# Kernel optimization log

Hardware: AMD Instinct MI355X
Metric: run time of the kernel (lower is better)

The kernel has to match this reference:

```python
import jax, jax.numpy as jnp
import numpy as np

B, S, D, H = 64, 512, 512, 1024


def setup_inputs() -> dict:
    key = jax.random.key(0)
    ks = jax.random.split(key, 18)
    p = {}
    p["inputs"] = jax.random.normal(ks[0], (B, S, D), jnp.float32)
    p["H0"] = jax.random.normal(ks[1], (B, H), jnp.float32)
    p["C0"] = jax.random.normal(ks[2], (B, H), jnp.float32)
    INIT_STD = 0.01  # nn.initializers.normal() default stddev
    for j, n in enumerate(["i", "f", "o", "c"]):
        p[f"Wx{n}"] = INIT_STD * jax.random.normal(ks[3 + 3 * j], (D, H), jnp.float32)
        p[f"Wh{n}"] = INIT_STD * jax.random.normal(ks[4 + 3 * j], (H, H), jnp.float32)
        p[f"b{n}"] = jnp.zeros((H,), jnp.float32)
    # flax Dense default: lecun_normal kernel, zeros bias
    p["fc_W"] = jax.random.normal(ks[15], (H, 1), jnp.float32) / np.float32(np.sqrt(H))
    p["fc_b"] = jnp.zeros((1,), jnp.float32)
    return p


def _lstm_forward(inputs, H0, C0, Wxi, Whi, bi, Wxf, Whf, bf,
                  Wxo, Who, bo, Wxc, Whc, bc, fc_W, fc_b):
    # Fuse the 4 gate weight matrices: same math, one GEMM per source.
    Wx = jnp.concatenate([Wxi, Wxf, Wxo, Wxc], axis=1)  # [D, 4H]
    Wh = jnp.concatenate([Whi, Whf, Who, Whc], axis=1)  # [H, 4H]
    b = jnp.concatenate([bi, bf, bo, bc], axis=0)       # [4H]
    # Precompute input projections for all timesteps: [S, B, 4H]
    x_proj = jnp.einsum('bsd,dg->sbg', inputs, Wx) + b

    def step(carry, xp):
        Hs, Cs = carry
        g = xp + Hs @ Wh                       # [B, 4H]
        i, f, o, c = jnp.split(g, 4, axis=-1)
        i = jax.nn.sigmoid(i)
        f = jax.nn.sigmoid(f)
        o = jax.nn.sigmoid(o)
        c = jnp.tanh(c)
        Cn = f * Cs + i * c
        Hn = o * jnp.tanh(Cn)
        return (Hn, Cn), Hn

    (Hf, Cf), outs = jax.lax.scan(step, (H0, C0), x_proj)
    outputs = jnp.transpose(outs, (1, 0, 2))   # [B, S, H]
    pred = outputs @ fc_W + fc_b               # [B, S, 1]
    return pred, Hf, Cf


def reference(inputs, H0, C0, Wxi, Whi, bi, Wxf, Whf, bf,
              Wxo, Who, bo, Wxc, Whc, bc, fc_W, fc_b):
    return _lstm_forward(inputs, H0, C0, Wxi, Whi, bi, Wxf, Whf, bf,
                         Wxo, Who, bo, Wxc, Whc, bc, fc_W, fc_b)
```

## Files before the change

### kernel.cpp

```cpp
#include <hip/hip_runtime.h>

typedef unsigned short u16;
typedef __bf16 bf16x8 __attribute__((ext_vector_type(8)));
typedef float f32x4 __attribute__((ext_vector_type(4)));

#define NWG 256

__device__ __forceinline__ u16 f2bf(float f) {
  union { float f; unsigned u; } v; v.f = f;
  unsigned r = v.u + 0x7fffu + ((v.u >> 16) & 1u);
  return (u16)(r >> 16);
}
__device__ __forceinline__ float bf2f(u16 h) {
  union { unsigned u; float f; } v; v.u = ((unsigned)h) << 16;
  return v.f;
}
__device__ __forceinline__ float fsig(float x) { return 1.0f / (1.0f + __expf(-x)); }
__device__ __forceinline__ float ftanh(float x) {
  float a = fabsf(x);
  float e = __expf(2.0f * a);
  float t = 1.0f - 2.0f / (e + 1.0f);
  return copysignf(t, x);
}

__global__ __launch_bounds__(256) void k_cvt_in(const float* __restrict__ inp,
                                                u16* __restrict__ dst) {
  unsigned i = blockIdx.x * 256 + threadIdx.x;
  unsigned d8 = i & 63u;
  unsigned b = (i >> 6) & 63u;
  unsigned s = i >> 12;
  const float* src = inp + ((size_t)b * 512 + s) * 512 + (size_t)d8 * 8;
  float4 x0 = *(const float4*)src;
  float4 x1 = *(const float4*)(src + 4);
  union { u16 h[8]; uint4 v; } o;
  o.h[0] = f2bf(x0.x); o.h[1] = f2bf(x0.y); o.h[2] = f2bf(x0.z); o.h[3] = f2bf(x0.w);
  o.h[4] = f2bf(x1.x); o.h[5] = f2bf(x1.y); o.h[6] = f2bf(x1.z); o.h[7] = f2bf(x1.w);
  *(uint4*)(dst + ((size_t)s * 64 + b) * 512 + d8 * 8) = o.v;
}

__global__ __launch_bounds__(256) void k_cvt_w(const float* __restrict__ W0,
                                               const float* __restrict__ W1,
                                               const float* __restrict__ W2,
                                               const float* __restrict__ W3,
                                               int K, u16* __restrict__ dst) {
  unsigned i = blockIdx.x * 256 + threadIdx.x;
  unsigned kb = (unsigned)K >> 3;
  unsigned k8 = i % kb;
  unsigned n = i / kb;
  if (n >= 4096) return;
  unsigned gate = n >> 10, h = n & 1023u;
  const float* W = (gate == 0) ? W0 : (gate == 1) ? W1 : (gate == 2) ? W2 : W3;
  union { u16 hh[8]; uint4 v; } o;
#pragma unroll
  for (int q = 0; q < 8; ++q) o.hh[q] = f2bf(W[(size_t)(k8 * 8 + q) * 1024 + h]);
  *(uint4*)(dst + (size_t)n * K + k8 * 8) = o.v;
}

__global__ __launch_bounds__(256) void k_init(const float* __restrict__ H0,
                                              u16* __restrict__ hbuf,
                                              unsigned* __restrict__ bar) {
  unsigned i = blockIdx.x * 256 + threadIdx.x;
  if (i < 16384) bar[i] = 0u;
  if (i < 65536) hbuf[i] = f2bf(H0[i]);
}

__global__ __launch_bounds__(256) void k_xp(const u16* __restrict__ A,
                                            const u16* __restrict__ Bm,
                                            u16* __restrict__ Xp) {
  __shared__ u16 Al[64][72];
  __shared__ u16 Bl[64][72];
  int t = threadIdx.x;
  int lane = t & 63, wid = t >> 6;
  int m0 = blockIdx.x * 64, n0 = blockIdx.y * 64;
  int quad = lane >> 4, l15 = lane & 15;
  f32x4 acc[4];
#pragma unroll
  for (int i = 0; i < 4; ++i) acc[i] = (f32x4){0.f, 0.f, 0.f, 0.f};
  int srow = t >> 2, sk = (t & 3) * 16;
  for (int kc = 0; kc < 512; kc += 64) {
    const u16* s1 = A + (size_t)(m0 + srow) * 512 + kc + sk;
    *(uint4*)&Al[srow][sk] = *(const uint4*)s1;
    *(uint4*)&Al[srow][sk + 8] = *(const uint4*)(s1 + 8);
    const u16* s2 = Bm + (size_t)(n0 + srow) * 512 + kc + sk;
    *(uint4*)&Bl[srow][sk] = *(const uint4*)s2;
    *(uint4*)&Bl[srow][sk + 8] = *(const uint4*)(s2 + 8);
    __syncthreads();
#pragma unroll
    for (int ks = 0; ks < 64; ks += 32) {
      bf16x8 a = *(const bf16x8*)&Al[wid * 16 + l15][ks + quad * 8];
#pragma unroll
      for (int nt = 0; nt < 4; ++nt) {
        bf16x8 b = *(const bf16x8*)&Bl[nt * 16 + l15][ks + quad * 8];
        acc[nt] = __builtin_amdgcn_mfma_f32_16x16x32_bf16(a, b, acc[nt], 0, 0, 0);
      }
    }
    __syncthreads();
  }
#pragma unroll
  for (int nt = 0; nt < 4; ++nt)
#pragma unroll
    for (int r = 0; r < 4; ++r) {
      size_t row = (size_t)m0 + wid * 16 + quad * 4 + r;
      Xp[row * 4096 + n0 + nt * 16 + l15] = f2bf(acc[nt][r]);
    }
}

__global__ __launch_bounds__(512, 2) void k_recur(
    u16* hbuf, const u16* __restrict__ whc, const u16* __restrict__ wxc,
    const u16* xp, const u16* inpb, const float* __restrict__ C0,
    const float* __restrict__ bi, const float* __restrict__ bff,
    const float* __restrict__ bo, const float* __restrict__ bc,
    float* __restrict__ dout, unsigned* bar, int use_xp) {
  int t = threadIdx.x;
  int wg = blockIdx.x;
  int lane = t & 63;
  int wid = t >> 6;
  int kset = wid >> 2;
  int wm = wid & 3;
  int h0 = wg << 2;
  int quad = lane >> 4;
  int ncol = lane & 15;

  unsigned* flags = bar;

  __shared__ u16 wxl[16][520];
  __shared__ float gt[2][4][16][17];
  __shared__ float biasl[16];

  int gate = ncol >> 2, j = ncol & 3;
  size_t colg = (size_t)gate * 1024 + h0 + j;
  bf16x8 wreg[16];
  {
    const u16* wb = whc + colg * 1024 + kset * 512 + quad * 8;
#pragma unroll
    for (int kk = 0; kk < 16; ++kk) wreg[kk] = *(const bf16x8*)(wb + kk * 32);
  }
  if (!use_xp) {
    int n = t >> 5;
    int part = t & 31;
    int g2 = n >> 2, j2n = n & 3;
    size_t cg = (size_t)g2 * 1024 + h0 + j2n;
    const u16* src2 = wxc + cg * 512 + part * 16;
#pragma unroll
    for (int q = 0; q < 2; ++q)
      *(uint4*)&wxl[n][part * 16 + q * 8] = *(const uint4*)(src2 + q * 8);
  }
  if (t < 16) {
    int g3 = t >> 2, j3 = t & 3;
    const float* bp = (g3 == 0) ? bi : (g3 == 1) ? bff : (g3 == 2) ? bo : bc;
    biasl[t] = bp[h0 + j3];
  }
  float Creg0 = 0.f, Creg1 = 0.f;
  if (t < 128) {
    int b = t >> 1, j2 = (t & 1) * 2;
    Creg0 = C0[b * 1024 + h0 + j2];
    Creg1 = C0[b * 1024 + h0 + j2 + 1];
  }

  int brow = wm * 16 + ncol;

  u16 xn0 = 0, xn1 = 0, xn2 = 0, xn3 = 0;
  const u16* xpc = 0;
  if (use_xp) {
    xpc = xp + (size_t)(wm * 16 + quad * 4) * 4096 + gate * 1024 + h0 + j;
    if (kset == 0) {
      xn0 = xpc[0]; xn1 = xpc[4096]; xn2 = xpc[8192]; xn3 = xpc[12288];
    }
  }
  __syncthreads();

  for (int s = 0; s < 512; ++s) {
    f32x4 acc = (f32x4){0.f, 0.f, 0.f, 0.f};
    f32x4 acc2 = (f32x4){0.f, 0.f, 0.f, 0.f};
    const u16* hrow = hbuf + (size_t)s * 65536 + (size_t)brow * 1024 + kset * 512;
    if (use_xp) {
      if (kset == 0) {
        acc[0] = bf2f(xn0); acc[1] = bf2f(xn1);
        acc[2] = bf2f(xn2); acc[3] = bf2f(xn3);
      }
    } else {
      const u16* irow = inpb + (size_t)s * 32768 + (size_t)brow * 512;
#pragma unroll
      for (int kk = 0; kk < 8; ++kk) {
        int kb = kset * 256 + kk * 32 + quad * 8;
        bf16x8 a = *(const bf16x8*)(irow + kb);
        bf16x8 w = *(const bf16x8*)&wxl[ncol][kb];
        acc = __builtin_amdgcn_mfma_f32_16x16x32_bf16(a, w, acc, 0, 0, 0);
      }
    }
#pragma unroll
    for (int kk = 0; kk < 16; ++kk) {
      bf16x8 a = *(const bf16x8*)(hrow + kk * 32 + quad * 8);
      if (kk & 1)
        acc2 = __builtin_amdgcn_mfma_f32_16x16x32_bf16(a, wreg[kk], acc2, 0, 0, 0);
      else
        acc = __builtin_amdgcn_mfma_f32_16x16x32_bf16(a, wreg[kk], acc, 0, 0, 0);
    }
    acc += acc2;
#pragma unroll
    for (int r = 0; r < 4; ++r)
      gt[kset][wm][quad * 4 + r][ncol] = acc[r];
    __syncthreads();
    if (t < 128) {
      int b = t >> 1, j2 = (t & 1) * 2;
      int m = b & 15, w2 = b >> 4;
      float Hn[2], Cn[2];
#pragma unroll
      for (int e = 0; e < 2; ++e) {
        int jj = j2 + e;
        float gi = gt[0][w2][m][jj] + gt[1][w2][m][jj] + biasl[jj];
        float gf = gt[0][w2][m][4 + jj] + gt[1][w2][m][4 + jj] + biasl[4 + jj];
        float go_ = gt[0][w2][m][8 + jj] + gt[1][w2][m][8 + jj] + biasl[8 + jj];
        float gc = gt[0][w2][m][12 + jj] + gt[1][w2][m][12 + jj] + biasl[12 + jj];
        float iv = fsig(gi), fv = fsig(gf), ov = fsig(go_), cv = ftanh(gc);
        float Cp = e ? Creg1 : Creg0;
        Cn[e] = fv * Cp + iv * cv;
        Hn[e] = ov * ftanh(Cn[e]);
      }
      Creg0 = Cn[0];
      Creg1 = Cn[1];
      unsigned pack = (unsigned)f2bf(Hn[0]) | ((unsigned)f2bf(Hn[1]) << 16);
      unsigned* hp = (unsigned*)(hbuf + (size_t)(s + 1) * 65536 + b * 1024 + h0 + j2);
      __hip_atomic_store(hp, pack, __ATOMIC_RELAXED, __HIP_MEMORY_SCOPE_AGENT);
      if (s == 511) {
        dout[32768 + b * 1024 + h0 + j2] = Hn[0];
        dout[32768 + b * 1024 + h0 + j2 + 1] = Hn[1];
        dout[98304 + b * 1024 + h0 + j2] = Cn[0];
        dout[98304 + b * 1024 + h0 + j2 + 1] = Cn[1];
      }
    }
    unsigned s1 = (unsigned)(s + 1);
    __syncthreads();
    if (s1 < 512) {
      if (t == 0)
        __hip_atomic_store(&flags[wg * 32], s1, __ATOMIC_RELAXED,
                           __HIP_MEMORY_SCOPE_AGENT);
      if (use_xp && kset == 0) {
        const u16* xpp = xpc + (size_t)s1 * 262144;
        xn0 = xpp[0]; xn1 = xpp[4096]; xn2 = xpp[8192]; xn3 = xpp[12288];
      }
      __asm__ volatile("" ::: "memory");
      if (t < 256) {
        while (__hip_atomic_load(&flags[t * 32], __ATOMIC_RELAXED,
                                 __HIP_MEMORY_SCOPE_AGENT) < s1)
          __builtin_amdgcn_s_sleep(2);
      }
      __syncthreads();
    }
  }
}

__global__ __launch_bounds__(256) void k_pred(const u16* __restrict__ hbuf,
                                              const float* __restrict__ fcW,
                                              const float* __restrict__ fcb,
                                              float* __restrict__ out) {
  __shared__ float w[1024];
  int t = threadIdx.x;
#pragma unroll
  for (int i = 0; i < 4; ++i) w[t + i * 256] = fcW[t + i * 256];
  __syncthreads();
  int wid = t >> 6, lane = t & 63;
  int row = blockIdx.x * 4 + wid;
  int b = row >> 9, s = row & 511;
  const u16* h = hbuf + (size_t)(s + 1) * 65536 + (size_t)b * 1024;
  float sum = 0.f;
#pragma unroll
  for (int it = 0; it < 16; ++it) {
    int hh = it * 64 + lane;
    sum += bf2f(h[hh]) * w[hh];
  }
#pragma unroll
  for (int o = 32; o > 0; o >>= 1) sum += __shfl_down(sum, o, 64);
  if (lane == 0) out[row] = sum + fcb[0];
}

extern "C" void kernel_launch(void* const* d_in, const int* in_sizes, int n_in,
                              void* d_out, int out_size, void* d_ws, size_t ws_size,
                              hipStream_t stream) {
  const float* inputs = (const float*)d_in[0];
  const float* H0 = (const float*)d_in[1];
  const float* C0 = (const float*)d_in[2];
  const float* Wxi = (const float*)d_in[3];
  const float* Whi = (const float*)d_in[4];
  const float* bi = (const float*)d_in[5];
  const float* Wxf = (const float*)d_in[6];
  const float* Whf = (const float*)d_in[7];
  const float* bff = (const float*)d_in[8];
  const float* Wxo = (const float*)d_in[9];
  const float* Who = (const float*)d_in[10];
  const float* bo = (const float*)d_in[11];
  const float* Wxc = (const float*)d_in[12];
  const float* Whc = (const float*)d_in[13];
  const float* bc = (const float*)d_in[14];
  const float* fcW = (const float*)d_in[15];
  const float* fcb = (const float*)d_in[16];
  float* out = (float*)d_out;

  char* ws = (char*)d_ws;
  size_t off = 0;
  auto take = [&](size_t bytes) {
    char* p = ws + off;
    off += (bytes + 255) & ~(size_t)255;
    return p;
  };
  unsigned* bar = (unsigned*)take(16384 * 4);
  u16* inpb = (u16*)take((size_t)512 * 64 * 512 * 2);
  u16* wxcT = (u16*)take((size_t)4096 * 512 * 2);
  u16* whcT = (u16*)take((size_t)4096 * 1024 * 2);
  u16* hbuf = (u16*)take((size_t)513 * 64 * 1024 * 2);
  u16* xpb = (u16*)take((size_t)32768 * 4096 * 2);
  size_t needA = off;
  int useA = (ws_size >= needA) ? 1 : 0;

  k_cvt_in<<<8192, 256, 0, stream>>>(inputs, inpb);
  k_cvt_w<<<1024, 256, 0, stream>>>(Wxi, Wxf, Wxo, Wxc, 512, wxcT);
  k_cvt_w<<<2048, 256, 0, stream>>>(Whi, Whf, Who, Whc, 1024, whcT);
  k_init<<<256, 256, 0, stream>>>(H0, hbuf, bar);
  if (useA) k_xp<<<dim3(512, 64), 256, 0, stream>>>(inpb, wxcT, xpb);
  k_recur<<<NWG, 512, 0, stream>>>(hbuf, whcT, wxcT, xpb, inpb, C0, bi, bff, bo,
                                   bc, out, bar, useA);
  k_pred<<<8192, 256, 0, stream>>>(hbuf, fcW, fcb, out);
}
```

Measured before the change: 4.062 ms.

## Split recurrence into batch groups with per-group barriers and full-K per wave

Repartitions the recurrent kernel so each group of 32 workgroups owns 8 batch rows, and each wave holds the full-K slice of Wh for 4 hidden columns in registers. Gate sums are no longer split across two K halves, so the intra-block syncthreads before the cell update is dropped and each wave does its own cell update. The cross-workgroup barrier now waits only on the 32 workgroups in the same batch group instead of all 256. The trade-off is half of each MFMA tile wasted (only 8 of 16 rows used), more weight registers per lane, and the use_xp flag becoming a template parameter.

```diff
diff --git a/kernel.cpp b/kernel.cpp
--- a/kernel.cpp
+++ b/kernel.cpp
@@ -105,129 +105,120 @@
     }
 }
 
+template <int USE_XP>
 __global__ __launch_bounds__(512, 2) void k_recur(
     u16* hbuf, const u16* __restrict__ whc, const u16* __restrict__ wxc,
     const u16* xp, const u16* inpb, const float* __restrict__ C0,
     const float* __restrict__ bi, const float* __restrict__ bff,
     const float* __restrict__ bo, const float* __restrict__ bc,
-    float* __restrict__ dout, unsigned* bar, int use_xp) {
+    float* __restrict__ dout, unsigned* bar) {
   int t = threadIdx.x;
   int wg = blockIdx.x;
+  int g = wg >> 5;
+  int wgi = wg & 31;
   int lane = t & 63;
-  int wid = t >> 6;
-  int kset = wid >> 2;
-  int wm = wid & 3;
-  int h0 = wg << 2;
+  int w = t >> 6;
   int quad = lane >> 4;
   int ncol = lane & 15;
+  int gate = ncol >> 2, hcl = ncol & 3;
+  int hc0 = wgi * 32 + w * 4;
 
   unsigned* flags = bar;
 
-  __shared__ u16 wxl[16][520];
-  __shared__ float gt[2][4][16][17];
-  __shared__ float biasl[16];
-
-  int gate = ncol >> 2, j = ncol & 3;
-  size_t colg = (size_t)gate * 1024 + h0 + j;
-  bf16x8 wreg[16];
+  __shared__ float gt[8][8][17];
+  __shared__ float biasl[8][16];
+
+  int n = gate * 1024 + hc0 + hcl;
+  bf16x8 wreg[32];
   {
-    const u16* wb = whc + colg * 1024 + kset * 512 + quad * 8;
-#pragma unroll
-    for (int kk = 0; kk < 16; ++kk) wreg[kk] = *(const bf16x8*)(wb + kk * 32);
-  }
-  if (!use_xp) {
-    int n = t >> 5;
-    int part = t & 31;
-    int g2 = n >> 2, j2n = n & 3;
-    size_t cg = (size_t)g2 * 1024 + h0 + j2n;
-    const u16* src2 = wxc + cg * 512 + part * 16;
-#pragma unroll
-    for (int q = 0; q < 2; ++q)
-      *(uint4*)&wxl[n][part * 16 + q * 8] = *(const uint4*)(src2 + q * 8);
-  }
-  if (t < 16) {
-    int g3 = t >> 2, j3 = t & 3;
-    const float* bp = (g3 == 0) ? bi : (g3 == 1) ? bff : (g3 == 2) ? bo : bc;
-    biasl[t] = bp[h0 + j3];
-  }
-  float Creg0 = 0.f, Creg1 = 0.f;
-  if (t < 128) {
-    int b = t >> 1, j2 = (t & 1) * 2;
-    Creg0 = C0[b * 1024 + h0 + j2];
-    Creg1 = C0[b * 1024 + h0 + j2 + 1];
-  }
-
-  int brow = wm * 16 + ncol;
+    const u16* wb = whc + (size_t)n * 1024 + quad * 8;
+#pragma unroll
+    for (int ks = 0; ks < 32; ++ks) wreg[ks] = *(const bf16x8*)(wb + ks * 32);
+  }
+  bf16x8 wxreg[USE_XP ? 1 : 16];
+  if (!USE_XP) {
+    const u16* wb2 = wxc + (size_t)n * 512 + quad * 8;
+#pragma unroll
+    for (int ks = 0; ks < 16; ++ks) wxreg[ks] = *(const bf16x8*)(wb2 + ks * 32);
+  }
+  if (lane < 16) {
+    const float* bp = (gate == 0) ? bi : (gate == 1) ? bff : (gate == 2) ? bo : bc;
+    biasl[w][lane] = bp[hc0 + hcl];
+  }
+  int bl = (lane & 31) >> 2, jcl = lane & 3;
+  int bg = 8 * g + bl;
+  int hcg = hc0 + jcl;
+  float Creg = 0.f;
+  if (lane < 32) Creg = C0[bg * 1024 + hcg];
+
+  int ba = 8 * g + (ncol & 7);
 
   u16 xn0 = 0, xn1 = 0, xn2 = 0, xn3 = 0;
   const u16* xpc = 0;
-  if (use_xp) {
-    xpc = xp + (size_t)(wm * 16 + quad * 4) * 4096 + gate * 1024 + h0 + j;
-    if (kset == 0) {
+  if (USE_XP) {
+    xpc = xp + (size_t)(8 * g + quad * 4) * 4096 + n;
+    if (quad < 2) {
       xn0 = xpc[0]; xn1 = xpc[4096]; xn2 = xpc[8192]; xn3 = xpc[12288];
     }
   }
   __syncthreads();
 
+  const u16* hrow = hbuf + (size_t)ba * 1024 + quad * 8;
   for (int s = 0; s < 512; ++s) {
     f32x4 acc = (f32x4){0.f, 0.f, 0.f, 0.f};
     f32x4 acc2 = (f32x4){0.f, 0.f, 0.f, 0.f};
-    const u16* hrow = hbuf + (size_t)s * 65536 + (size_t)brow * 1024 + kset * 512;
-    if (use_xp) {
-      if (kset == 0) {
+    if (USE_XP) {
+      if (quad < 2) {
         acc[0] = bf2f(xn0); acc[1] = bf2f(xn1);
         acc[2] = bf2f(xn2); acc[3] = bf2f(xn3);
       }
     } else {
-      const u16* irow = inpb + (size_t)s * 32768 + (size_t)brow * 512;
-#pragma unroll
-      for (int kk = 0; kk < 8; ++kk) {
-        int kb = kset * 256 + kk * 32 + quad * 8;
-        bf16x8 a = *(const bf16x8*)(irow + kb);
-        bf16x8 w = *(const bf16x8*)&wxl[ncol][kb];
-        acc = __builtin_amdgcn_mfma_f32_16x16x32_bf16(a, w, acc, 0, 0, 0);
-      }
-    }
-#pragma unroll
-    for (int kk = 0; kk < 16; ++kk) {
-      bf16x8 a = *(const bf16x8*)(hrow + kk * 32 + quad * 8);
-      if (kk & 1)
-        acc2 = __builtin_amdgcn_mfma_f32_16x16x32_bf16(a, wreg[kk], acc2, 0, 0, 0);
+      const u16* irow = inpb + (size_t)s * 32768 + (size_t)ba * 512 + quad * 8;
+#pragma unroll
+      for (int ks = 0; ks < 16; ++ks) {
+        bf16x8 a = *(const bf16x8*)(irow + ks * 32);
+        if (ks & 1)
+          acc2 = __builtin_amdgcn_mfma_f32_16x16x32_bf16(a, wxreg[ks], acc2, 0, 0, 0);
+        else
+          acc = __builtin_amdgcn_mfma_f32_16x16x32_bf16(a, wxreg[ks], acc, 0, 0, 0);
+      }
+    }
+#pragma unroll
+    for (int ks = 0; ks < 32; ++ks) {
+      bf16x8 a = *(const bf16x8*)(hrow + ks * 32);
+      if (ks & 1)
+        acc2 = __builtin_amdgcn_mfma_f32_16x16x32_bf16(a, wreg[ks], acc2, 0, 0, 0);
       else
-        acc = __builtin_amdgcn_mfma_f32_16x16x32_bf16(a, wreg[kk], acc, 0, 0, 0);
+        acc = __builtin_amdgcn_mfma_f32_16x16x32_bf16(a, wreg[ks], acc, 0, 0, 0);
     }
     acc += acc2;
-#pragma unroll
-    for (int r = 0; r < 4; ++r)
-      gt[kset][wm][quad * 4 + r][ncol] = acc[r];
-    __syncthreads();
-    if (t < 128) {
-      int b = t >> 1, j2 = (t & 1) * 2;
-      int m = b & 15, w2 = b >> 4;
-      float Hn[2], Cn[2];
-#pragma unroll
-      for (int e = 0; e < 2; ++e) {
-        int jj = j2 + e;
-        float gi = gt[0][w2][m][jj] + gt[1][w2][m][jj] + biasl[jj];
-        float gf = gt[0][w2][m][4 + jj] + gt[1][w2][m][4 + jj] + biasl[4 + jj];
-        float go_ = gt[0][w2][m][8 + jj] + gt[1][w2][m][8 + jj] + biasl[8 + jj];
-        float gc = gt[0][w2][m][12 + jj] + gt[1][w2][m][12 + jj] + biasl[12 + jj];
-        float iv = fsig(gi), fv = fsig(gf), ov = fsig(go_), cv = ftanh(gc);
-        float Cp = e ? Creg1 : Creg0;
-        Cn[e] = fv * Cp + iv * cv;
-        Hn[e] = ov * ftanh(Cn[e]);
-      }
-      Creg0 = Cn[0];
-      Creg1 = Cn[1];
-      unsigned pack = (unsigned)f2bf(Hn[0]) | ((unsigned)f2bf(Hn[1]) << 16);
-      unsigned* hp = (unsigned*)(hbuf + (size_t)(s + 1) * 65536 + b * 1024 + h0 + j2);
+    hrow += 65536;
+    if (quad < 2) {
+#pragma unroll
+      for (int r = 0; r < 4; ++r) gt[w][quad * 4 + r][ncol] = acc[r];
+    }
+    float Hn = 0.f, Cn = 0.f;
+    if (lane < 32) {
+      float gi = gt[w][bl][jcl] + biasl[w][jcl];
+      float gf = gt[w][bl][4 + jcl] + biasl[w][4 + jcl];
+      float go_ = gt[w][bl][8 + jcl] + biasl[w][8 + jcl];
+      float gc = gt[w][bl][12 + jcl] + biasl[w][12 + jcl];
+      float iv = fsig(gi), fv = fsig(gf), ov = fsig(go_), cv = ftanh(gc);
+      Cn = fv * Creg + iv * cv;
+      Creg = Cn;
+      Hn = ov * ftanh(Cn);
+    }
+    unsigned hb = (unsigned)f2bf(Hn);
+    unsigned up = (unsigned)__shfl_down((int)hb, 1, 64);
+    if (lane < 32 && (jcl & 1) == 0) {
+      unsigned pack = hb | (up << 16);
+      unsigned* hp =
+          (unsigned*)(hbuf + (size_t)(s + 1) * 65536 + bg * 1024 + hcg);
       __hip_atomic_store(hp, pack, __ATOMIC_RELAXED, __HIP_MEMORY_SCOPE_AGENT);
-      if (s == 511) {
-        dout[32768 + b * 1024 + h0 + j2] = Hn[0];
-        dout[32768 + b * 1024 + h0 + j2 + 1] = Hn[1];
-        dout[98304 + b * 1024 + h0 + j2] = Cn[0];
-        dout[98304 + b * 1024 + h0 + j2 + 1] = Cn[1];
-      }
+    }
+    if (s == 511 && lane < 32) {
+      dout[32768 + bg * 1024 + hcg] = Hn;
+      dout[98304 + bg * 1024 + hcg] = Cn;
     }
     unsigned s1 = (unsigned)(s + 1);
     __syncthreads();
@@ -235,15 +226,15 @@
       if (t == 0)
         __hip_atomic_store(&flags[wg * 32], s1, __ATOMIC_RELAXED,
                            __HIP_MEMORY_SCOPE_AGENT);
-      if (use_xp && kset == 0) {
+      if (USE_XP && quad < 2) {
         const u16* xpp = xpc + (size_t)s1 * 262144;
         xn0 = xpp[0]; xn1 = xpp[4096]; xn2 = xpp[8192]; xn3 = xpp[12288];
       }
       __asm__ volatile("" ::: "memory");
-      if (t < 256) {
-        while (__hip_atomic_load(&flags[t * 32], __ATOMIC_RELAXED,
+      if (t < 32) {
+        while (__hip_atomic_load(&flags[(g * 32 + t) * 32], __ATOMIC_RELAXED,
                                  __HIP_MEMORY_SCOPE_AGENT) < s1)
-          __builtin_amdgcn_s_sleep(2);
+          __builtin_amdgcn_s_sleep(1);
       }
       __syncthreads();
     }
@@ -254,10 +245,10 @@
                                               const float* __restrict__ fcW,
                                               const float* __restrict__ fcb,
                                               float* __restrict__ out) {
-  __shared__ float w[1024];
+  __shared__ float wsm[1024];
   int t = threadIdx.x;
 #pragma unroll
-  for (int i = 0; i < 4; ++i) w[t + i * 256] = fcW[t + i * 256];
+  for (int i = 0; i < 4; ++i) wsm[t + i * 256] = fcW[t + i * 256];
   __syncthreads();
   int wid = t >> 6, lane = t & 63;
   int row = blockIdx.x * 4 + wid;
@@ -267,7 +258,7 @@
 #pragma unroll
   for (int it = 0; it < 16; ++it) {
     int hh = it * 64 + lane;
-    sum += bf2f(h[hh]) * w[hh];
+    sum += bf2f(h[hh]) * wsm[hh];
   }
 #pragma unroll
   for (int o = 32; o > 0; o >>= 1) sum += __shfl_down(sum, o, 64);
@@ -316,8 +307,13 @@
   k_cvt_w<<<1024, 256, 0, stream>>>(Wxi, Wxf, Wxo, Wxc, 512, wxcT);
   k_cvt_w<<<2048, 256, 0, stream>>>(Whi, Whf, Who, Whc, 1024, whcT);
   k_init<<<256, 256, 0, stream>>>(H0, hbuf, bar);
-  if (useA) k_xp<<<dim3(512, 64), 256, 0, stream>>>(inpb, wxcT, xpb);
-  k_recur<<<NWG, 512, 0, stream>>>(hbuf, whcT, wxcT, xpb, inpb, C0, bi, bff, bo,
-                                   bc, out, bar, useA);
+  if (useA) {
+    k_xp<<<dim3(512, 64), 256, 0, stream>>>(inpb, wxcT, xpb);
+    k_recur<1><<<NWG, 512, 0, stream>>>(hbuf, whcT, wxcT, xpb, inpb, C0, bi, bff,
+                                        bo, bc, out, bar);
+  } else {
+    k_recur<0><<<NWG, 512, 0, stream>>>(hbuf, whcT, wxcT, xpb, inpb, C0, bi, bff,
+                                        bo, bc, out, bar);
+  }
   k_pred<<<8192, 256, 0, stream>>>(hbuf, fcW, fcb, out);
 }
```

Measured after the change: 6.289 ms. 54.8% more time.
